# Optimization experiments

Hardware: AMD Instinct MI355X
Metric: run time of the kernel (lower is better)

The kernel has to match this reference:

```python
import jax, jax.numpy as jnp
import numpy as np

K = 20  # hard-coded in DGCNN.__init__

def _pd_neg(x):
    # negative squared pairwise distance, [B,N,C] -> [B,N,N]
    inner = jnp.einsum('bnc,bmc->bnm', x, x)
    sq = jnp.sum(x * x, axis=-1)
    return 2.0 * inner - sq[:, :, None] - sq[:, None, :]

def _knn(x):
    return jax.lax.top_k(_pd_neg(x), K)[1]  # [B,N,K]

def _edge_feat(x, idx):
    # x: [B,N,C], idx: [B,N,K] -> [B,N,K,2C] = concat(central, neighbor-central)
    nb = jax.vmap(lambda p, i: p[i])(x, idx)
    c = x[:, :, None, :]
    return jnp.concatenate([jnp.broadcast_to(c, nb.shape), nb - c], axis=-1)

def _conv(x, w, b, act=True):
    # 1x1 Conv2d == per-point linear; BN at inference with init stats is identity
    y = jnp.einsum('...c,cd->...d', x, w) + b
    return jax.nn.relu(y) if act else y

def _forward(x, tw1, tb1, tw2, tb2, tw3, tb3, tfw1, tfb1, tfw2, tfb2, txw, txb,
             e1w1, e1b1, e1w2, e1b2, e2w1, e2b1, e2w2, e2b2, e3w1, e3b1,
             c1w, c1b, c2w, c2b, c3w, c3b, c4w, c4b):
    pts = x[:, :, :3]
    # spatial transform net on edge features of raw xyz
    ef = _edge_feat(pts, _knn(pts))                      # [B,N,K,6]
    t = _conv(_conv(ef, tw1, tb1), tw2, tb2)
    t = jnp.max(t, axis=2)                               # max over neighbors
    t = _conv(t, tw3, tb3)                               # [B,N,1024]
    t = jnp.max(t, axis=1)                               # global maxpool -> [B,1024]
    t = jax.nn.relu(t @ tfw1 + tfb1)
    t = jax.nn.relu(t @ tfw2 + tfb2)
    xf = (t @ txw + txb).reshape(-1, 3, 3)
    p = jnp.einsum('bnc,bcd->bnd', pts, xf)              # transformed points
    # EdgeConv 1
    ef = _edge_feat(p, _knn(p))                          # [B,N,K,6]
    x1 = jnp.max(_conv(_conv(ef, e1w1, e1b1), e1w2, e1b2), axis=2)   # [B,N,64]
    # EdgeConv 2
    ef = _edge_feat(x1, _knn(x1))                        # [B,N,K,128]
    x2 = jnp.max(_conv(_conv(ef, e2w1, e2b1), e2w2, e2b2), axis=2)
    # EdgeConv 3
    ef = _edge_feat(x2, _knn(x2))
    x3 = jnp.max(_conv(ef, e3w1, e3b1), axis=2)
    # global feature + per-point head
    net = _conv(jnp.concatenate([x1, x2, x3], axis=-1), c1w, c1b)    # [B,N,1024]
    g = jnp.max(net, axis=1, keepdims=True)              # maxpool over all points
    g = jnp.broadcast_to(g, (g.shape[0], x1.shape[1], g.shape[2]))
    net = jnp.concatenate([g, x1, x2, x3], axis=-1)      # [B,N,1216]
    net = _conv(net, c2w, c2b)
    net = _conv(net, c3w, c3b)
    # dropout is identity at inference (training=False)
    return _conv(net, c4w, c4b, act=False)               # [B,N,num_classes]

def setup_inputs():
    keys = iter(jax.random.split(jax.random.key(0), 64))
    def w(*shape):
        return jax.random.normal(next(keys), shape, jnp.float32) / np.float32(np.sqrt(shape[0]))
    def b(n):
        return 0.01 * jax.random.normal(next(keys), (n,), jnp.float32)
    B, N, F = 4, 4096, 6
    d = dict(x=jax.random.normal(next(keys), (B, N, F), jnp.float32))
    d.update(tw1=w(6, 64), tb1=b(64), tw2=w(64, 128), tb2=b(128), tw3=w(128, 1024), tb3=b(1024),
             tfw1=w(1024, 512), tfb1=b(512), tfw2=w(512, 256), tfb2=b(256),
             txw=0.01 * w(256, 9), txb=jnp.eye(3, dtype=jnp.float32).reshape(9))
    d.update(e1w1=w(6, 64), e1b1=b(64), e1w2=w(64, 64), e1b2=b(64),
             e2w1=w(128, 64), e2b1=b(64), e2w2=w(64, 64), e2b2=b(64),
             e3w1=w(128, 64), e3b1=b(64))
    d.update(c1w=w(192, 1024), c1b=b(1024), c2w=w(1216, 512), c2b=b(512),
             c3w=w(512, 256), c3b=b(256), c4w=w(256, 2), c4b=b(2))
    return d

def reference(x, tw1, tb1, tw2, tb2, tw3, tb3, tfw1, tfb1, tfw2, tfb2, txw, txb,
              e1w1, e1b1, e1w2, e1b2, e2w1, e2b1, e2w2, e2b2, e3w1, e3b1,
              c1w, c1b, c2w, c2b, c3w, c3b, c4w, c4b):
    return _forward(x, tw1, tb1, tw2, tb2, tw3, tb3, tfw1, tfb1, tfw2, tfb2, txw, txb,
                    e1w1, e1b1, e1w2, e1b2, e2w1, e2b1, e2w2, e2b2, e3w1, e3b1,
                    c1w, c1b, c2w, c2b, c3w, c3b, c4w, c4b)
```

## Files before the change

kernel.cpp:

```cpp
#include <hip/hip_runtime.h>

#define Nn 4096
#define KK 20
#define BN 16384

typedef __attribute__((ext_vector_type(8))) short bf16x8;
typedef __attribute__((ext_vector_type(4))) float f32x4;

__device__ __forceinline__ unsigned short f2bf(float f) {
  unsigned int x = __float_as_uint(f);
  return (unsigned short)((x + 0x7fffu + ((x >> 16) & 1u)) >> 16);
}
__device__ __forceinline__ float bf2f(unsigned short u) {
  return __uint_as_float(((unsigned int)u) << 16);
}

#define INS5(dd, tt)                                                         \
  if (dd > m5) {                                                             \
    if (dd > m3) {                                                           \
      if (dd > m1) { m5=m4;t5=t4; m4=m3;t4=t3; m3=m2;t3=t2; m2=m1;t2=t1; m1=dd;t1=tt; } \
      else if (dd > m2) { m5=m4;t5=t4; m4=m3;t4=t3; m3=m2;t3=t2; m2=dd;t2=tt; } \
      else { m5=m4;t5=t4; m4=m3;t4=t3; m3=dd;t3=tt; }                        \
    } else if (dd > m4) { m5=m4;t5=t4; m4=dd;t4=tt; }                        \
    else { m5=dd; t5=tt; }                                                   \
  }

__global__ void k_pts(const float* __restrict__ x, float* __restrict__ pts) {
  int i = blockIdx.x * 256 + threadIdx.x;
  if (i < BN * 3) {
    int pt = i / 3, c = i - 3 * pt;
    pts[i] = x[pt * 6 + c];
  }
}

__global__ void k_cvtT(const float* __restrict__ src, unsigned short* __restrict__ dst,
                       int N, int K, int ldn, int row0) {
  int i = blockIdx.x * 256 + threadIdx.x;
  if (i >= N * K) return;
  int n = i / K, k = i - n * K;
  dst[i] = f2bf(src[(size_t)(row0 + k) * ldn + n]);
}

__global__ void k_cvtT3(const float* __restrict__ src, unsigned short* __restrict__ h,
                        unsigned short* __restrict__ m, unsigned short* __restrict__ l,
                        int N, int K, int ldn) {
  int i = blockIdx.x * 256 + threadIdx.x;
  if (i >= N * K) return;
  int n = i / K, k = i - n * K;
  float x = src[(size_t)k * ldn + n];
  unsigned short hh = f2bf(x); float xh = bf2f(hh);
  unsigned short mm = f2bf(x - xh); float xm = bf2f(mm);
  unsigned short ll = f2bf(x - xh - xm);
  h[i] = hh; m[i] = mm; l[i] = ll;
}

__global__ void k_tv3(const float* __restrict__ part, const float* __restrict__ bias,
                      unsigned short* __restrict__ h, unsigned short* __restrict__ m,
                      unsigned short* __restrict__ l) {
  int i = blockIdx.x * 256 + threadIdx.x;
  if (i >= 16 * 1024) return;
  int row = i >> 10, col = i & 1023;
  float v = 0.f;
  if (row < 4) {
    float mx = -INFINITY;
#pragma unroll 8
    for (int s = 0; s < 32; ++s) mx = fmaxf(mx, part[((size_t)row * 32 + s) * 1024 + col]);
    v = fmaxf(mx + bias[col], 0.f);
  }
  unsigned short hh = f2bf(v); float xh = bf2f(hh);
  unsigned short mm = f2bf(v - xh); float xm = bf2f(mm);
  unsigned short ll = f2bf(v - xh - xm);
  h[i] = hh; m[i] = mm; l[i] = ll;
}

__global__ void k_pad3(const float* __restrict__ src, int rows, int cols,
                       unsigned short* __restrict__ h, unsigned short* __restrict__ m,
                       unsigned short* __restrict__ l) {
  int i = blockIdx.x * 256 + threadIdx.x;
  if (i >= 16 * cols) return;
  int row = i / cols, col = i - row * cols;
  float v = (row < rows) ? src[(size_t)row * cols + col] : 0.f;
  unsigned short hh = f2bf(v); float xh = bf2f(hh);
  unsigned short mm = f2bf(v - xh); float xm = bf2f(mm);
  unsigned short ll = f2bf(v - xh - xm);
  h[i] = hh; m[i] = mm; l[i] = ll;
}

template <int N, int K, int SEG>
__global__ __launch_bounds__(256) void k_gemmSK(const unsigned short* __restrict__ Ah,
                                                const unsigned short* __restrict__ Am,
                                                const unsigned short* __restrict__ Al,
                                                const unsigned short* __restrict__ Bh,
                                                const unsigned short* __restrict__ Bm,
                                                const unsigned short* __restrict__ Bl,
                                                float* __restrict__ partial) {
  constexpr int KSEG = K / SEG;
  constexpr int KS = KSEG / 32;
  int t = threadIdx.x;
  int wv = t >> 6, lane = t & 63;
  int quad = lane >> 4, l16 = lane & 15;
  int bx = blockIdx.x;
  int nb = bx / SEG, seg = bx - nb * SEG;
  int col = nb * 64 + wv * 16 + l16;
  int k0 = seg * KSEG;
  size_t wo = (size_t)col * K + k0 + quad * 8;
  size_t ao = (size_t)l16 * K + k0 + quad * 8;
  f32x4 acc = {0.f, 0.f, 0.f, 0.f};
#pragma unroll
  for (int s = 0; s < KS; ++s) {
    bf16x8 xh = *(const bf16x8*)(Ah + ao + s * 32);
    bf16x8 xm = *(const bf16x8*)(Am + ao + s * 32);
    bf16x8 xl = *(const bf16x8*)(Al + ao + s * 32);
    bf16x8 wh = *(const bf16x8*)(Bh + wo + s * 32);
    bf16x8 wm = *(const bf16x8*)(Bm + wo + s * 32);
    bf16x8 wl = *(const bf16x8*)(Bl + wo + s * 32);
    acc = __builtin_amdgcn_mfma_f32_16x16x32_bf16(xh, wh, acc, 0, 0, 0);
    acc = __builtin_amdgcn_mfma_f32_16x16x32_bf16(xh, wm, acc, 0, 0, 0);
    acc = __builtin_amdgcn_mfma_f32_16x16x32_bf16(xm, wh, acc, 0, 0, 0);
    acc = __builtin_amdgcn_mfma_f32_16x16x32_bf16(xh, wl, acc, 0, 0, 0);
    acc = __builtin_amdgcn_mfma_f32_16x16x32_bf16(xl, wh, acc, 0, 0, 0);
    acc = __builtin_amdgcn_mfma_f32_16x16x32_bf16(xm, wm, acc, 0, 0, 0);
  }
  if (quad == 0) {
#pragma unroll
    for (int r = 0; r < 4; ++r)
      partial[((size_t)seg * 4 + r) * N + col] = acc[r];
  }
}

__global__ void k_redS(const float* __restrict__ partial, const float* __restrict__ bias,
                       float* __restrict__ outp, int N, int SEG, int relu) {
  int i = blockIdx.x * 256 + threadIdx.x;
  if (i >= 4 * N) return;
  int r = i / N, c = i - r * N;
  float s = 0.f;
  for (int seg = 0; seg < SEG; ++seg) s += partial[((size_t)seg * 4 + r) * N + c];
  if (bias) s += bias[c];
  if (relu) s = fmaxf(s, 0.f);
  outp[(size_t)r * N + c] = s;
}

__global__ __launch_bounds__(256) void k_fc3p(const float* __restrict__ h2, const float* __restrict__ txw,
                                              const float* __restrict__ txb, const float* __restrict__ pts,
                                              float* __restrict__ p) {
  __shared__ float sh2[256];
  __shared__ float sxf[9];
  int t = threadIdx.x;
  int b = blockIdx.x;
  sh2[t] = h2[(size_t)b * 256 + t];
  __syncthreads();
  if (t < 9) {
    float acc = txb[t];
    for (int j = 0; j < 256; ++j) acc = fmaf(sh2[j], txw[j * 9 + t], acc);
    sxf[t] = acc;
  }
  __syncthreads();
  for (int n = t; n < Nn; n += 256) {
    const float* pr = pts + ((size_t)b * Nn + n) * 3;
    float a0 = pr[0], a1 = pr[1], a2 = pr[2];
    float* po = p + ((size_t)b * Nn + n) * 3;
#pragma unroll
    for (int d = 0; d < 3; ++d) po[d] = a0 * sxf[d] + a1 * sxf[3 + d] + a2 * sxf[6 + d];
  }
}

__device__ __forceinline__ float dist4(const float4* __restrict__ tile4, int c,
                                       float qx, float qy, float qz, float qsq) {
  float4 v = tile4[c];
  float dot = fmaf(qx, v.x, fmaf(qy, v.y, qz * v.z));
  return 2.0f * dot - qsq - v.w;
}

__global__ __launch_bounds__(1024) void k_knn3(const float* __restrict__ src, int* __restrict__ idx) {
  __shared__ float4 tile4[Nn];
  int t = threadIdx.x;
  int wave = t >> 6, lane = t & 63;
  int g = blockIdx.x * 16 + wave;
  int b = g >> 12, n = g & (Nn - 1);
  const float* base = src + (size_t)b * Nn * 3;
  for (int e = t; e < Nn; e += 1024) {
    float x = base[e * 3], y = base[e * 3 + 1], z = base[e * 3 + 2];
    tile4[e] = make_float4(x, y, z, fmaf(x, x, fmaf(y, y, z * z)));
  }
  __syncthreads();
  float4 q4 = tile4[n];
  float qx = q4.x, qy = q4.y, qz = q4.z, qsq = q4.w;
  float m1 = -INFINITY, m2 = -INFINITY, m3 = -INFINITY, m4 = -INFINITY, m5 = -INFINITY;
  int t1 = 0, t2 = 0, t3 = 0, t4 = 0, t5 = 0;
#pragma unroll 4
  for (int tt = 0; tt < 64; ++tt) {
    float dd = dist4(tile4, (tt << 6) + lane, qx, qy, qz, qsq);
    INS5(dd, tt)
  }
  unsigned long long removed = 0ull;
  int cnt = 5;
  int sel = 0;
#pragma unroll 1
  for (int k = 0; k < 20; ++k) {
    float v = m1; int ci = (t1 << 6) | lane;
    float mx = v;
#pragma unroll
    for (int off = 32; off; off >>= 1) mx = fmaxf(mx, __shfl_xor(mx, off, 64));
    int cand = (v == mx) ? ci : 0x7FFFFFFF;
#pragma unroll
    for (int off = 32; off; off >>= 1) cand = min(cand, __shfl_xor(cand, off, 64));
    if (k == lane) sel = cand;
    if (cand == ci) {
      removed |= 1ull << t1;
      if (cnt > 1) { m1 = m2; t1 = t2; m2 = m3; t2 = t3; m3 = m4; t3 = t4; m4 = m5; t4 = t5; --cnt; }
      else {
        m1 = -INFINITY; m2 = -INFINITY; m3 = -INFINITY; m4 = -INFINITY; m5 = -INFINITY;
        t1 = 0; t2 = 0; t3 = 0; t4 = 0; t5 = 0;
#pragma unroll 1
        for (int tt = 0; tt < 64; ++tt) {
          if ((removed >> tt) & 1ull) continue;
          float dd = dist4(tile4, (tt << 6) + lane, qx, qy, qz, qsq);
          INS5(dd, tt)
        }
        cnt = 5;
      }
    }
  }
  if (lane < 20) idx[(size_t)g * KK + lane] = sel;
}

__global__ void k_sqnorm(const float* __restrict__ src, float* __restrict__ out) {
  int g = blockIdx.x * 256 + threadIdx.x;
  if (g >= BN) return;
  const float4* r = (const float4*)(src + (size_t)g * 64);
  float s = 0.f;
#pragma unroll
  for (int j = 0; j < 16; ++j) { float4 v = r[j]; s += v.x * v.x + v.y * v.y + v.z * v.z + v.w * v.w; }
  out[g] = s;
}

__device__ __forceinline__ void topk_d5(const float (&d)[64],
                                        float m1, int t1, float m2, int t2, float m3, int t3,
                                        float m4, int t4, float m5, int t5,
                                        int lane, int* __restrict__ op) {
  unsigned long long removed = 0ull;
  int cnt = 5;
  int sel = 0;
#pragma unroll 1
  for (int k = 0; k < 20; ++k) {
    float v = m1; int ci = (t1 << 6) | lane;
    float mx = v;
#pragma unroll
    for (int off = 32; off; off >>= 1) mx = fmaxf(mx, __shfl_xor(mx, off, 64));
    int cand = (v == mx) ? ci : 0x7FFFFFFF;
#pragma unroll
    for (int off = 32; off; off >>= 1) cand = min(cand, __shfl_xor(cand, off, 64));
    if (k == lane) sel = cand;
    if (cand == ci) {
      removed |= 1ull << t1;
      if (cnt > 1) { m1 = m2; t1 = t2; m2 = m3; t2 = t3; m3 = m4; t3 = t4; m4 = m5; t4 = t5; --cnt; }
      else {
        m1 = -INFINITY; m2 = -INFINITY; m3 = -INFINITY; m4 = -INFINITY; m5 = -INFINITY;
        t1 = 0; t2 = 0; t3 = 0; t4 = 0; t5 = 0;
#pragma unroll 1
        for (int tt = 0; tt < 64; ++tt) {
          if ((removed >> tt) & 1ull) continue;
          float dd = d[tt];
          INS5(dd, tt)
        }
        cnt = 5;
      }
    }
  }
  if (lane < 20) op[lane] = sel;
}

__global__ __launch_bounds__(1024) void k_dsel(const unsigned short* __restrict__ Xh,
                                               const unsigned short* __restrict__ Xm,
                                               const unsigned short* __restrict__ Xl,
                                               const float* __restrict__ sq,
                                               int* __restrict__ idx) {
  __shared__ float sD[16 * 1028];
  int t = threadIdx.x;
  int wave = t >> 6, lane = t & 63;
  int quad = lane >> 4, l16 = lane & 15;
  int blk = blockIdx.x;
  int b = blk >> 8, rs = blk & 255;
  int r0 = rs * 16;
  const size_t base = (size_t)b * Nn * 64;
  const float* sqb = sq + b * Nn;
  bf16x8 ah[2], am[2], al[2];
#pragma unroll
  for (int ks = 0; ks < 2; ++ks) {
    size_t ra = base + (size_t)(r0 + l16) * 64 + ks * 32 + quad * 8;
    ah[ks] = *(const bf16x8*)(Xh + ra);
    am[ks] = *(const bf16x8*)(Xm + ra);
    al[ks] = *(const bf16x8*)(Xl + ra);
  }
  float sqr[4];
#pragma unroll
  for (int r = 0; r < 4; ++r) sqr[r] = sqb[r0 + quad * 4 + r];
  float d[64];
  float m1 = -INFINITY, m2 = -INFINITY, m3 = -INFINITY, m4 = -INFINITY, m5 = -INFINITY;
  int t1 = 0, t2 = 0, t3 = 0, t4 = 0, t5 = 0;
#pragma unroll
  for (int ch = 0; ch < 4; ++ch) {
#pragma unroll
    for (int tt = 0; tt < 4; ++tt) {
      int cc = wave * 64 + tt * 16;
      int cb = ch * 1024 + cc;
      f32x4 acc = {0.f, 0.f, 0.f, 0.f};
#pragma unroll
      for (int ks = 0; ks < 2; ++ks) {
        size_t rb = base + (size_t)(cb + l16) * 64 + ks * 32 + quad * 8;
        bf16x8 bh = *(const bf16x8*)(Xh + rb);
        bf16x8 bm = *(const bf16x8*)(Xm + rb);
        bf16x8 bl = *(const bf16x8*)(Xl + rb);
        acc = __builtin_amdgcn_mfma_f32_16x16x32_bf16(ah[ks], bh, acc, 0, 0, 0);
        acc = __builtin_amdgcn_mfma_f32_16x16x32_bf16(ah[ks], bm, acc, 0, 0, 0);
        acc = __builtin_amdgcn_mfma_f32_16x16x32_bf16(am[ks], bh, acc, 0, 0, 0);
        acc = __builtin_amdgcn_mfma_f32_16x16x32_bf16(ah[ks], bl, acc, 0, 0, 0);
        acc = __builtin_amdgcn_mfma_f32_16x16x32_bf16(al[ks], bh, acc, 0, 0, 0);
        acc = __builtin_amdgcn_mfma_f32_16x16x32_bf16(am[ks], bm, acc, 0, 0, 0);
      }
      float sqc = sqb[cb + l16];
#pragma unroll
      for (int r = 0; r < 4; ++r)
        sD[(quad * 4 + r) * 1028 + cc + l16] = 2.0f * acc[r] - sqr[r] - sqc;
    }
    __syncthreads();
#pragma unroll
    for (int jj = 0; jj < 16; ++jj) {
      int tt = ch * 16 + jj;
      float dd = sD[wave * 1028 + jj * 64 + lane];
      d[tt] = dd;
      INS5(dd, tt)
    }
    __syncthreads();
  }
  topk_d5(d, m1, t1, m2, t2, m3, t3, m4, t4, m5, t5, lane,
          idx + (size_t)(b * Nn + r0 + wave) * KK);
}

__global__ __launch_bounds__(256) void k_uv3(const float* __restrict__ pts, const float* __restrict__ w1,
                                             const float* __restrict__ b1, float* __restrict__ uvb) {
  __shared__ float sw[384];
  __shared__ float sb[64];
  int t = threadIdx.x;
  for (int e = t; e < 384; e += 256) sw[e] = w1[e];
  if (t < 64) sb[t] = b1[t];
  __syncthreads();
  int pl = t >> 6, c = t & 63;
  int p = blockIdx.x * 4 + pl;
  const float* pr = pts + (size_t)p * 3;
  float x0 = pr[0], x1 = pr[1], x2 = pr[2];
  float wb0 = sw[192 + c], wb1 = sw[256 + c], wb2 = sw[320 + c];
  float v = x0 * wb0 + x1 * wb1 + x2 * wb2;
  float u = sb[c] + x0 * (sw[c] - wb0) + x1 * (sw[64 + c] - wb1) + x2 * (sw[128 + c] - wb2);
  uvb[(size_t)p * 128 + c] = u;
  uvb[(size_t)p * 128 + 64 + c] = v;
}

__global__ void k_prepD(const float* __restrict__ w1, float* __restrict__ Md) {
  int i = blockIdx.x * 256 + threadIdx.x;
  if (i >= 8192) return;
  int j = i >> 7, c = i & 127;
  Md[i] = (c < 64) ? (w1[j * 64 + c] - w1[(64 + j) * 64 + c]) : w1[(64 + j) * 64 + (c - 64)];
}

__global__ __launch_bounds__(256) void k_uv(const float* __restrict__ x2, const float* __restrict__ Md,
                                            const float* __restrict__ bias, float* __restrict__ uv) {
  __shared__ float sM[8192];
  __shared__ float sx[32 * 68];
  int t = threadIdx.x;
  for (int e = t; e < 8192; e += 256) sM[e] = Md[e];
  int p0 = blockIdx.x * 32;
  for (int e = t; e < 512; e += 256) {
    int r = e >> 4, c4 = e & 15;
    *(float4*)(sx + r * 68 + c4 * 4) = *(const float4*)(x2 + (size_t)(p0 + r) * 64 + c4 * 4);
  }
  __syncthreads();
  int c = t & 127, rg = t >> 7;
  float badd = (c < 64) ? bias[c] : 0.f;
  float accv[16];
#pragma unroll
  for (int r = 0; r < 16; ++r) accv[r] = 0.f;
#pragma unroll
  for (int jc = 0; jc < 8; ++jc) {
    float mreg[8];
#pragma unroll
    for (int q = 0; q < 8; ++q) mreg[q] = sM[(jc * 8 + q) * 128 + c];
#pragma unroll
    for (int r = 0; r < 16; ++r) {
      const float* xr = sx + (rg * 16 + r) * 68 + jc * 8;
      float4 a = *(const float4*)xr, bb = *(const float4*)(xr + 4);
      float s = accv[r];
      s = fmaf(a.x, mreg[0], s); s = fmaf(a.y, mreg[1], s);
      s = fmaf(a.z, mreg[2], s); s = fmaf(a.w, mreg[3], s);
      s = fmaf(bb.x, mreg[4], s); s = fmaf(bb.y, mreg[5], s);
      s = fmaf(bb.z, mreg[6], s); s = fmaf(bb.w, mreg[7], s);
      accv[r] = s;
    }
  }
#pragma unroll
  for (int r = 0; r < 16; ++r)
    uv[(size_t)(p0 + rg * 16 + r) * 128 + c] = accv[r] + badd;
}

template <int NOUT, bool WRITEF, bool SPLIT3, bool CAT>
__global__ __launch_bounds__(256, 4) void k_econv(const float* __restrict__ uv,
                                                  const int* __restrict__ idx,
                                                  const unsigned short* __restrict__ W2h,
                                                  const unsigned short* __restrict__ W2m,
                                                  const unsigned short* __restrict__ W2l,
                                                  const float* __restrict__ b2,
                                                  float* __restrict__ outF,
                                                  unsigned short* __restrict__ oh,
                                                  unsigned short* __restrict__ om,
                                                  unsigned short* __restrict__ ol,
                                                  unsigned short* __restrict__ ocat,
                                                  int catoff) {
  __shared__ unsigned short y3[4][3][20 * 72];
  int t = threadIdx.x;
  int wv = t >> 6, lane = t & 63;
  int quad = lane >> 4, l16 = lane & 15;
  int p0 = blockIdx.x * 4;
  int p = p0 + wv;
  size_t nbase = (size_t)(p >> 12) * Nn;
  constexpr int CT = NOUT / 64;
  bf16x8 wfh[CT][2], wfm[CT][2], wfl[CT][2];
#pragma unroll
  for (int ct = 0; ct < CT; ++ct)
#pragma unroll
    for (int ks = 0; ks < 2; ++ks) {
      size_t wo = (size_t)(wv * (CT * 16) + ct * 16 + l16) * 64 + ks * 32 + quad * 8;
      wfh[ct][ks] = *(const bf16x8*)(W2h + wo);
      wfm[ct][ks] = *(const bf16x8*)(W2m + wo);
      wfl[ct][ks] = *(const bf16x8*)(W2l + wo);
    }
  const int* ip = idx + (size_t)p * KK;
  float u = uv[(size_t)p * 128 + lane];
  unsigned short* yh = y3[wv][0];
  unsigned short* ym = y3[wv][1];
  unsigned short* yl = y3[wv][2];
  float vv[20];
#pragma unroll
  for (int k = 0; k < 20; ++k) {
    int nb = ip[k];
    vv[k] = uv[(nbase + nb) * 128 + 64 + lane];
  }
#pragma unroll
  for (int k = 0; k < 20; ++k) {
    float y = fmaxf(u + vv[k], 0.f);
    unsigned short hh = f2bf(y); float fh = bf2f(hh);
    unsigned short mm = f2bf(y - fh); float fm = bf2f(mm);
    unsigned short ll = f2bf(y - fh - fm);
    yh[k * 72 + lane] = hh;
    ym[k * 72 + lane] = mm;
    yl[k * 72 + lane] = ll;
  }
  __syncthreads();
#pragma unroll 1
  for (int pp = 0; pp < 4; ++pp) {
    const unsigned short* ph0 = y3[pp][0];
    const unsigned short* pm0 = y3[pp][1];
    const unsigned short* pl0 = y3[pp][2];
    f32x4 acc[CT][2];
#pragma unroll
    for (int ct = 0; ct < CT; ++ct) {
      acc[ct][0] = (f32x4){0.f, 0.f, 0.f, 0.f};
      acc[ct][1] = (f32x4){0.f, 0.f, 0.f, 0.f};
    }
#pragma unroll
    for (int ks = 0; ks < 2; ++ks) {
      bf16x8 ah[2], am[2], al[2];
#pragma unroll
      for (int mt = 0; mt < 2; ++mt) {
        int row = mt * 16 + l16;
        int rr = (row < 20) ? row : 0;
        int aoff = rr * 72 + ks * 32 + quad * 8;
        ah[mt] = *(const bf16x8*)(ph0 + aoff);
        am[mt] = *(const bf16x8*)(pm0 + aoff);
        al[mt] = *(const bf16x8*)(pl0 + aoff);
      }
#pragma unroll
      for (int ct = 0; ct < CT; ++ct)
#pragma unroll
        for (int mt = 0; mt < 2; ++mt) {
          f32x4 a = acc[ct][mt];
          a = __builtin_amdgcn_mfma_f32_16x16x32_bf16(ah[mt], wfh[ct][ks], a, 0, 0, 0);
          a = __builtin_amdgcn_mfma_f32_16x16x32_bf16(ah[mt], wfm[ct][ks], a, 0, 0, 0);
          a = __builtin_amdgcn_mfma_f32_16x16x32_bf16(am[mt], wfh[ct][ks], a, 0, 0, 0);
          a = __builtin_amdgcn_mfma_f32_16x16x32_bf16(ah[mt], wfl[ct][ks], a, 0, 0, 0);
          a = __builtin_amdgcn_mfma_f32_16x16x32_bf16(al[mt], wfh[ct][ks], a, 0, 0, 0);
// ... 62 lines not shown
#pragma unroll
  for (int s = 0; s < KS; ++s) bfr[s] = *(const bf16x8*)(wrow + s * 32);
  const unsigned short* Ab = A + ((size_t)b * Nn + ns * 128 + l16) * K + quad * 8;
  float rmax = -INFINITY;
#pragma unroll 2
  for (int mt = 0; mt < 8; ++mt) {
    const unsigned short* ar = Ab + (size_t)mt * 16 * K;
    f32x4 acc = {0.f, 0.f, 0.f, 0.f};
#pragma unroll
    for (int s = 0; s < KS; ++s) {
      bf16x8 af = *(const bf16x8*)(ar + s * 32);
      acc = __builtin_amdgcn_mfma_f32_16x16x32_bf16(af, bfr[s], acc, 0, 0, 0);
    }
    rmax = fmaxf(rmax, fmaxf(fmaxf(acc[0], acc[1]), fmaxf(acc[2], acc[3])));
  }
  rmax = fmaxf(rmax, __shfl_xor(rmax, 16, 64));
  rmax = fmaxf(rmax, __shfl_xor(rmax, 32, 64));
  if (quad == 0) outp[((size_t)b * 32 + ns) * 1024 + n0 + l16] = rmax;
}

template <int K>
__global__ __launch_bounds__(256) void k_mgemm3s(const unsigned short* __restrict__ Ah,
                                                 const unsigned short* __restrict__ Am,
                                                 const unsigned short* __restrict__ Al,
                                                 const unsigned short* __restrict__ Bh,
                                                 const unsigned short* __restrict__ Bm,
                                                 const unsigned short* __restrict__ Bl,
                                                 float* __restrict__ outp) {
  constexpr int KS = K / 32;
  int t = threadIdx.x;
  int wv = t >> 6, lane = t & 63;
  int quad = lane >> 4, l16 = lane & 15;
  int blk = blockIdx.x;
  int b = blk >> 9, cb = (blk >> 5) & 15, ns = blk & 31;
  int n0 = cb * 64 + wv * 16;
  bf16x8 wh[KS], wm[KS], wl[KS];
  size_t wo = (size_t)(n0 + l16) * K + quad * 8;
#pragma unroll
  for (int s = 0; s < KS; ++s) {
    wh[s] = *(const bf16x8*)(Bh + wo + s * 32);
    wm[s] = *(const bf16x8*)(Bm + wo + s * 32);
    wl[s] = *(const bf16x8*)(Bl + wo + s * 32);
  }
  size_t ao = ((size_t)b * Nn + ns * 128 + l16) * K + quad * 8;
  float rmax = -INFINITY;
#pragma unroll 1
  for (int mt = 0; mt < 8; ++mt) {
    size_t ar = ao + (size_t)mt * 16 * K;
    f32x4 acc = {0.f, 0.f, 0.f, 0.f};
#pragma unroll
    for (int s = 0; s < KS; ++s) {
      bf16x8 xh = *(const bf16x8*)(Ah + ar + s * 32);
      bf16x8 xm = *(const bf16x8*)(Am + ar + s * 32);
      bf16x8 xl = *(const bf16x8*)(Al + ar + s * 32);
      acc = __builtin_amdgcn_mfma_f32_16x16x32_bf16(xh, wh[s], acc, 0, 0, 0);
      acc = __builtin_amdgcn_mfma_f32_16x16x32_bf16(xh, wm[s], acc, 0, 0, 0);
      acc = __builtin_amdgcn_mfma_f32_16x16x32_bf16(xm, wh[s], acc, 0, 0, 0);
      acc = __builtin_amdgcn_mfma_f32_16x16x32_bf16(xh, wl[s], acc, 0, 0, 0);
      acc = __builtin_amdgcn_mfma_f32_16x16x32_bf16(xl, wh[s], acc, 0, 0, 0);
      acc = __builtin_amdgcn_mfma_f32_16x16x32_bf16(xm, wm[s], acc, 0, 0, 0);
    }
    rmax = fmaxf(rmax, fmaxf(fmaxf(acc[0], acc[1]), fmaxf(acc[2], acc[3])));
  }
  rmax = fmaxf(rmax, __shfl_xor(rmax, 16, 64));
  rmax = fmaxf(rmax, __shfl_xor(rmax, 32, 64));
  if (quad == 0) outp[((size_t)b * 32 + ns) * 1024 + n0 + l16] = rmax;
}

__global__ __launch_bounds__(256) void k_final(const unsigned short* __restrict__ xcat,
                                               const float* __restrict__ gc,
                                               const float* __restrict__ c2b,
                                               const unsigned short* __restrict__ c2wT,
                                               const unsigned short* __restrict__ c3wT,
                                               const float* __restrict__ c3b,
                                               const float* __restrict__ c4w, const float* __restrict__ c4b,
                                               float* __restrict__ out) {
  __shared__ unsigned short z5[16 * 520];
  __shared__ float z2[16 * 260];
  int t = threadIdx.x;
  int wv = t >> 6, lane = t & 63;
  int quad = lane >> 4, l16 = lane & 15;
  int p0 = blockIdx.x * 16;
  int b = p0 >> 12;
  bf16x8 a1[6];
  const unsigned short* ar = xcat + (size_t)(p0 + l16) * 192 + quad * 8;
#pragma unroll
  for (int s = 0; s < 6; ++s) a1[s] = *(const bf16x8*)(ar + s * 32);
#pragma unroll 1
  for (int ntw = 0; ntw < 8; ++ntw) {
    int col = wv * 128 + ntw * 16 + l16;
    float bias = gc[(size_t)b * 512 + col] + c2b[col];
    f32x4 acc = {bias, bias, bias, bias};
    const unsigned short* wr = c2wT + (size_t)col * 192 + quad * 8;
#pragma unroll
    for (int s = 0; s < 6; ++s) {
      bf16x8 bfr = *(const bf16x8*)(wr + s * 32);
      acc = __builtin_amdgcn_mfma_f32_16x16x32_bf16(a1[s], bfr, acc, 0, 0, 0);
    }
#pragma unroll
    for (int r = 0; r < 4; ++r)
      z5[(quad * 4 + r) * 520 + col] = f2bf(fmaxf(acc[r], 0.f));
  }
  __syncthreads();
  bf16x8 a2[16];
#pragma unroll
  for (int s = 0; s < 16; ++s) a2[s] = *(const bf16x8*)(z5 + l16 * 520 + s * 32 + quad * 8);
#pragma unroll 1
  for (int ntw = 0; ntw < 4; ++ntw) {
    int col = wv * 64 + ntw * 16 + l16;
    float bias = c3b[col];
    f32x4 acc = {bias, bias, bias, bias};
    const unsigned short* wr = c3wT + (size_t)col * 512 + quad * 8;
#pragma unroll
    for (int s = 0; s < 16; ++s) {
      bf16x8 bfr = *(const bf16x8*)(wr + s * 32);
      acc = __builtin_amdgcn_mfma_f32_16x16x32_bf16(a2[s], bfr, acc, 0, 0, 0);
    }
#pragma unroll
    for (int r = 0; r < 4; ++r)
      z2[(quad * 4 + r) * 260 + col] = fmaxf(acc[r], 0.f);
  }
  __syncthreads();
  if (t < 32) {
    int m = t >> 1, e = t & 1;
    float acc = c4b[e];
    const float* zr = z2 + m * 260;
    for (int j = 0; j < 256; ++j) acc = fmaf(zr[j], c4w[j * 2 + e], acc);
    out[(size_t)(p0 + m) * 2 + e] = acc;
  }
}

extern "C" void kernel_launch(void* const* d_in, const int* in_sizes, int n_in,
                              void* d_out, int out_size, void* d_ws, size_t ws_size,
                              hipStream_t stream) {
  const float* xin = (const float*)d_in[0];
  const float* W[30];
  for (int i = 0; i < 30; ++i) W[i] = (const float*)d_in[i + 1];

  float* ws = (float*)d_ws;
  size_t off = 0;
  float* pts   = ws + off; off += (size_t)BN * 3;
  float* p     = ws + off; off += (size_t)BN * 3;
  int*   idx   = (int*)(ws + off); off += (size_t)BN * KK;
  float* sq    = ws + off; off += BN;
  float* dpart = ws + off; off += 4 * 32 * 1024;
  float* h1    = ws + off; off += 4 * 512;
  float* h2b   = ws + off; off += 4 * 256;
  float* x1    = ws + off; off += (size_t)BN * 64;
  float* x2    = ws + off; off += (size_t)BN * 64;
  float* gpart = ws + off; off += 4 * 32 * 1024;
  float* gc    = ws + off; off += 4 * 512;
  float* uvb   = ws + off; off += (size_t)BN * 128;
  float* partial = ws + off; off += 16 * 4 * 512;
  unsigned short* xcat = (unsigned short*)(ws + off); off += (size_t)BN * 96;
  unsigned short* c1wT = (unsigned short*)(ws + off); off += 98304;
  unsigned short* c2wT = (unsigned short*)(ws + off); off += 49152;
  unsigned short* c3wT = (unsigned short*)(ws + off); off += 65536;
  unsigned short* w3Th = (unsigned short*)(ws + off); off += 65536;
  unsigned short* w3Tm = (unsigned short*)(ws + off); off += 65536;
  unsigned short* w3Tl = (unsigned short*)(ws + off); off += 65536;
  unsigned short* tw2h = (unsigned short*)(ws + off); off += 4096;
  unsigned short* tw2m = (unsigned short*)(ws + off); off += 4096;
  unsigned short* tw2l = (unsigned short*)(ws + off); off += 4096;
  unsigned short* e1h  = (unsigned short*)(ws + off); off += 2048;
  unsigned short* e1m  = (unsigned short*)(ws + off); off += 2048;
  unsigned short* e1l  = (unsigned short*)(ws + off); off += 2048;
  unsigned short* e2h  = (unsigned short*)(ws + off); off += 2048;
  unsigned short* e2m  = (unsigned short*)(ws + off); off += 2048;
  unsigned short* e2l  = (unsigned short*)(ws + off); off += 2048;
  unsigned short* xsh  = (unsigned short*)(ws + off); off += 524288;
  unsigned short* xsm  = (unsigned short*)(ws + off); off += 524288;
  unsigned short* xsl  = (unsigned short*)(ws + off); off += 524288;
  float* MdC   = ws + off; off += 8192;
  float* MdD   = ws + off; off += 8192;
  unsigned short* fw1h = (unsigned short*)(ws + off); off += 262144;
  unsigned short* fw1m = (unsigned short*)(ws + off); off += 262144;
  unsigned short* fw1l = (unsigned short*)(ws + off); off += 262144;
  unsigned short* cw2h = (unsigned short*)(ws + off); off += 262144;
  unsigned short* cw2m = (unsigned short*)(ws + off); off += 262144;
  unsigned short* cw2l = (unsigned short*)(ws + off); off += 262144;
  unsigned short* fw2h = (unsigned short*)(ws + off); off += 65536;
  unsigned short* fw2m = (unsigned short*)(ws + off); off += 65536;
  unsigned short* fw2l = (unsigned short*)(ws + off); off += 65536;
  unsigned short* tvh  = (unsigned short*)(ws + off); off += 8192;
  unsigned short* tvm  = (unsigned short*)(ws + off); off += 8192;
  unsigned short* tvl  = (unsigned short*)(ws + off); off += 8192;
  unsigned short* h13h = (unsigned short*)(ws + off); off += 4096;
  unsigned short* h13m = (unsigned short*)(ws + off); off += 4096;
  unsigned short* h13l = (unsigned short*)(ws + off); off += 4096;
  float* Dbuf  = ws + off; off += (size_t)Nn * Nn;
  unsigned short* t3h = (unsigned short*)Dbuf;
  unsigned short* t3m = t3h + (size_t)BN * 128;
  unsigned short* t3l = t3m + (size_t)BN * 128;

  k_cvtT<<<dim3(768), dim3(256), 0, stream>>>(W[22], c1wT, 1024, 192, 1024, 0);
  k_cvtT<<<dim3(384), dim3(256), 0, stream>>>(W[24], c2wT, 512, 192, 512, 1024);
  k_cvtT<<<dim3(512), dim3(256), 0, stream>>>(W[26], c3wT, 256, 512, 256, 0);
  k_cvtT3<<<dim3(512), dim3(256), 0, stream>>>(W[4], w3Th, w3Tm, w3Tl, 1024, 128, 1024);
  k_cvtT3<<<dim3(32), dim3(256), 0, stream>>>(W[2], tw2h, tw2m, tw2l, 128, 64, 128);
  k_cvtT3<<<dim3(16), dim3(256), 0, stream>>>(W[14], e1h, e1m, e1l, 64, 64, 64);
  k_cvtT3<<<dim3(16), dim3(256), 0, stream>>>(W[18], e2h, e2m, e2l, 64, 64, 64);
  k_cvtT3<<<dim3(2048), dim3(256), 0, stream>>>(W[6], fw1h, fw1m, fw1l, 512, 1024, 512);
  k_cvtT3<<<dim3(2048), dim3(256), 0, stream>>>(W[24], cw2h, cw2m, cw2l, 512, 1024, 512);
  k_cvtT3<<<dim3(512), dim3(256), 0, stream>>>(W[8], fw2h, fw2m, fw2l, 256, 512, 256);
  k_prepD<<<dim3(32), dim3(256), 0, stream>>>(W[16], MdC);
  k_prepD<<<dim3(32), dim3(256), 0, stream>>>(W[20], MdD);

  k_pts<<<dim3(192), dim3(256), 0, stream>>>(xin, pts);

  k_knn3<<<dim3(1024), dim3(1024), 0, stream>>>(pts, idx);
  k_uv3<<<dim3(4096), dim3(256), 0, stream>>>(pts, W[0], W[1], uvb);
  k_econv<128, false, true, false><<<dim3(4096), dim3(256), 0, stream>>>(
      uvb, idx, tw2h, tw2m, tw2l, W[3], nullptr, t3h, t3m, t3l, nullptr, 0);
  k_mgemm3s<128><<<dim3(2048), dim3(256), 0, stream>>>(t3h, t3m, t3l, w3Th, w3Tm, w3Tl, dpart);
  k_tv3<<<dim3(64), dim3(256), 0, stream>>>(dpart, W[5], tvh, tvm, tvl);
  k_gemmSK<512, 1024, 16><<<dim3(128), dim3(256), 0, stream>>>(tvh, tvm, tvl, fw1h, fw1m, fw1l, partial);
  k_redS<<<dim3(8), dim3(256), 0, stream>>>(partial, W[7], h1, 512, 16, 1);
  k_pad3<<<dim3(32), dim3(256), 0, stream>>>(h1, 4, 512, h13h, h13m, h13l);
  k_gemmSK<256, 512, 8><<<dim3(32), dim3(256), 0, stream>>>(h13h, h13m, h13l, fw2h, fw2m, fw2l, partial);
  k_redS<<<dim3(4), dim3(256), 0, stream>>>(partial, W[9], h2b, 256, 8, 1);
  k_fc3p<<<dim3(4), dim3(256), 0, stream>>>(h2b, W[10], W[11], pts, p);

  k_knn3<<<dim3(1024), dim3(1024), 0, stream>>>(p, idx);
  k_uv3<<<dim3(4096), dim3(256), 0, stream>>>(p, W[12], W[13], uvb);
  k_econv<64, true, true, true><<<dim3(4096), dim3(256), 0, stream>>>(
      uvb, idx, e1h, e1m, e1l, W[15], x1, xsh, xsm, xsl, xcat, 0);
  k_sqnorm<<<dim3(64), dim3(256), 0, stream>>>(x1, sq);
  k_dsel<<<dim3(1024), dim3(1024), 0, stream>>>(xsh, xsm, xsl, sq, idx);
  k_uv<<<dim3(512), dim3(256), 0, stream>>>(x1, MdC, W[17], uvb);
  k_econv<64, true, true, true><<<dim3(4096), dim3(256), 0, stream>>>(
      uvb, idx, e2h, e2m, e2l, W[19], x2, xsh, xsm, xsl, xcat, 64);
  k_sqnorm<<<dim3(64), dim3(256), 0, stream>>>(x2, sq);
  k_dsel<<<dim3(1024), dim3(1024), 0, stream>>>(xsh, xsm, xsl, sq, idx);
  k_uv<<<dim3(512), dim3(256), 0, stream>>>(x2, MdD, W[21], uvb);
  k_gmax<<<dim3(4096), dim3(256), 0, stream>>>(uvb, idx, xcat);

  k_mgemm<192><<<dim3(2048), dim3(256), 0, stream>>>(xcat, c1wT, gpart);
  k_tv3<<<dim3(64), dim3(256), 0, stream>>>(gpart, W[23], tvh, tvm, tvl);
  k_gemmSK<512, 1024, 16><<<dim3(128), dim3(256), 0, stream>>>(tvh, tvm, tvl, cw2h, cw2m, cw2l, partial);
  k_redS<<<dim3(8), dim3(256), 0, stream>>>(partial, nullptr, gc, 512, 16, 0);
  k_final<<<dim3(1024), dim3(256), 0, stream>>>(xcat, gc, W[25], c2wT, c3wT,
                                                W[27], W[28], W[29], (float*)d_out);
}
```

Baseline: 1.276 ms.

## Split 64-dim kNN into column-quarter top-k kernels plus a merge pass

The fused distance and top-20 selection kernel for the 64-channel EdgeConv layers is replaced by two kernels. The first computes distances for 8 rows against a quarter of the columns in 512-thread blocks and writes per-quarter top-20 candidates. The second merges the 80 candidates per row into the final top-20. This adds parallelism, shrinks per-thread register arrays (16 instead of 64 values) and makes the rescan cheaper. In exchange, half the MFMA rows are wasted and candidates take an extra global round trip.

```diff
diff --git a/kernel.cpp b/kernel.cpp
--- a/kernel.cpp
+++ b/kernel.cpp
@@ -234,13 +234,70 @@
   out[g] = s;
 }
 
-__device__ __forceinline__ void topk_d5(const float (&d)[64],
-                                        float m1, int t1, float m2, int t2, float m3, int t3,
-                                        float m4, int t4, float m5, int t5,
-                                        int lane, int* __restrict__ op) {
-  unsigned long long removed = 0ull;
+__global__ __launch_bounds__(512) void k_dq(const unsigned short* __restrict__ Xh,
+                                            const unsigned short* __restrict__ Xm,
+                                            const unsigned short* __restrict__ Xl,
+                                            const float* __restrict__ sq,
+                                            float* __restrict__ cval,
+                                            int* __restrict__ cidx) {
+  __shared__ float sD[8 * 1028];
+  int t = threadIdx.x;
+  int wave = t >> 6, lane = t & 63;
+  int quad = lane >> 4, l16 = lane & 15;
+  int blk = blockIdx.x;
+  int b = blk >> 11, rs = (blk >> 2) & 511, qtr = blk & 3;
+  int r0 = rs * 8, q0 = qtr * 1024;
+  const size_t base = (size_t)b * Nn * 64;
+  const float* sqb = sq + b * Nn;
+  bf16x8 ah[2], am[2], al[2];
+#pragma unroll
+  for (int ks = 0; ks < 2; ++ks) {
+    size_t ra = base + (size_t)(r0 + (l16 & 7)) * 64 + ks * 32 + quad * 8;
+    ah[ks] = *(const bf16x8*)(Xh + ra);
+    am[ks] = *(const bf16x8*)(Xm + ra);
+    al[ks] = *(const bf16x8*)(Xl + ra);
+  }
+  float sqr[4];
+#pragma unroll
+  for (int r = 0; r < 4; ++r) sqr[r] = sqb[r0 + ((quad * 4 + r) & 7)];
+#pragma unroll
+  for (int tt = 0; tt < 8; ++tt) {
+    int cc = wave * 128 + tt * 16;
+    int cb = q0 + cc;
+    f32x4 acc = {0.f, 0.f, 0.f, 0.f};
+#pragma unroll
+    for (int ks = 0; ks < 2; ++ks) {
+      size_t rb = base + (size_t)(cb + l16) * 64 + ks * 32 + quad * 8;
+      bf16x8 bh = *(const bf16x8*)(Xh + rb);
+      bf16x8 bm = *(const bf16x8*)(Xm + rb);
+      bf16x8 bl = *(const bf16x8*)(Xl + rb);
+      acc = __builtin_amdgcn_mfma_f32_16x16x32_bf16(ah[ks], bh, acc, 0, 0, 0);
+      acc = __builtin_amdgcn_mfma_f32_16x16x32_bf16(ah[ks], bm, acc, 0, 0, 0);
+      acc = __builtin_amdgcn_mfma_f32_16x16x32_bf16(am[ks], bh, acc, 0, 0, 0);
+      acc = __builtin_amdgcn_mfma_f32_16x16x32_bf16(ah[ks], bl, acc, 0, 0, 0);
+      acc = __builtin_amdgcn_mfma_f32_16x16x32_bf16(al[ks], bh, acc, 0, 0, 0);
+      acc = __builtin_amdgcn_mfma_f32_16x16x32_bf16(am[ks], bm, acc, 0, 0, 0);
+    }
+    float sqc = sqb[cb + l16];
+    if (quad < 2) {
+#pragma unroll
+      for (int r = 0; r < 4; ++r)
+        sD[(quad * 4 + r) * 1028 + cc + l16] = 2.0f * acc[r] - sqr[r] - sqc;
+    }
+  }
+  __syncthreads();
+  float d[16];
+  float m1 = -INFINITY, m2 = -INFINITY, m3 = -INFINITY, m4 = -INFINITY, m5 = -INFINITY;
+  int t1 = 0, t2 = 0, t3 = 0, t4 = 0, t5 = 0;
+#pragma unroll
+  for (int jj = 0; jj < 16; ++jj) {
+    float dd = sD[wave * 1028 + jj * 64 + lane];
+    d[jj] = dd;
+    INS5(dd, jj)
+  }
+  unsigned removed = 0;
   int cnt = 5;
-  int sel = 0;
+  float selv = 0.f; int seli = 0;
 #pragma unroll 1
   for (int k = 0; k < 20; ++k) {
     float v = m1; int ci = (t1 << 6) | lane;
@@ -250,91 +307,59 @@
     int cand = (v == mx) ? ci : 0x7FFFFFFF;
 #pragma unroll
     for (int off = 32; off; off >>= 1) cand = min(cand, __shfl_xor(cand, off, 64));
-    if (k == lane) sel = cand;
+    if (k == lane) { selv = mx; seli = cand; }
     if (cand == ci) {
-      removed |= 1ull << t1;
+      removed |= 1u << t1;
       if (cnt > 1) { m1 = m2; t1 = t2; m2 = m3; t2 = t3; m3 = m4; t3 = t4; m4 = m5; t4 = t5; --cnt; }
       else {
         m1 = -INFINITY; m2 = -INFINITY; m3 = -INFINITY; m4 = -INFINITY; m5 = -INFINITY;
         t1 = 0; t2 = 0; t3 = 0; t4 = 0; t5 = 0;
-#pragma unroll 1
-        for (int tt = 0; tt < 64; ++tt) {
-          if ((removed >> tt) & 1ull) continue;
-          float dd = d[tt];
-          INS5(dd, tt)
+#pragma unroll
+        for (int tt = 0; tt < 16; ++tt) {
+          if (!((removed >> tt) & 1u)) {
+            float dd = d[tt];
+            INS5(dd, tt)
+          }
         }
         cnt = 5;
       }
     }
   }
-  if (lane < 20) op[lane] = sel;
-}
-
-__global__ __launch_bounds__(1024) void k_dsel(const unsigned short* __restrict__ Xh,
-                                               const unsigned short* __restrict__ Xm,
-                                               const unsigned short* __restrict__ Xl,
-                                               const float* __restrict__ sq,
-                                               int* __restrict__ idx) {
-  __shared__ float sD[16 * 1028];
+  if (lane < 20) {
+    size_t o = ((size_t)(b * Nn + r0 + wave) * 4 + qtr) * 20 + lane;
+    cval[o] = selv;
+    cidx[o] = q0 + seli;
+  }
+}
+
+__global__ __launch_bounds__(256) void k_dmerge(const float* __restrict__ cval,
+                                                const int* __restrict__ cidx,
+                                                int* __restrict__ idx) {
   int t = threadIdx.x;
   int wave = t >> 6, lane = t & 63;
-  int quad = lane >> 4, l16 = lane & 15;
-  int blk = blockIdx.x;
-  int b = blk >> 8, rs = blk & 255;
-  int r0 = rs * 16;
-  const size_t base = (size_t)b * Nn * 64;
-  const float* sqb = sq + b * Nn;
-  bf16x8 ah[2], am[2], al[2];
-#pragma unroll
-  for (int ks = 0; ks < 2; ++ks) {
-    size_t ra = base + (size_t)(r0 + l16) * 64 + ks * 32 + quad * 8;
-    ah[ks] = *(const bf16x8*)(Xh + ra);
-    am[ks] = *(const bf16x8*)(Xm + ra);
-    al[ks] = *(const bf16x8*)(Xl + ra);
-  }
-  float sqr[4];
-#pragma unroll
-  for (int r = 0; r < 4; ++r) sqr[r] = sqb[r0 + quad * 4 + r];
-  float d[64];
-  float m1 = -INFINITY, m2 = -INFINITY, m3 = -INFINITY, m4 = -INFINITY, m5 = -INFINITY;
-  int t1 = 0, t2 = 0, t3 = 0, t4 = 0, t5 = 0;
-#pragma unroll
-  for (int ch = 0; ch < 4; ++ch) {
-#pragma unroll
-    for (int tt = 0; tt < 4; ++tt) {
-      int cc = wave * 64 + tt * 16;
-      int cb = ch * 1024 + cc;
-      f32x4 acc = {0.f, 0.f, 0.f, 0.f};
-#pragma unroll
-      for (int ks = 0; ks < 2; ++ks) {
-        size_t rb = base + (size_t)(cb + l16) * 64 + ks * 32 + quad * 8;
-        bf16x8 bh = *(const bf16x8*)(Xh + rb);
-        bf16x8 bm = *(const bf16x8*)(Xm + rb);
-        bf16x8 bl = *(const bf16x8*)(Xl + rb);
-        acc = __builtin_amdgcn_mfma_f32_16x16x32_bf16(ah[ks], bh, acc, 0, 0, 0);
-        acc = __builtin_amdgcn_mfma_f32_16x16x32_bf16(ah[ks], bm, acc, 0, 0, 0);
-        acc = __builtin_amdgcn_mfma_f32_16x16x32_bf16(am[ks], bh, acc, 0, 0, 0);
-        acc = __builtin_amdgcn_mfma_f32_16x16x32_bf16(ah[ks], bl, acc, 0, 0, 0);
-        acc = __builtin_amdgcn_mfma_f32_16x16x32_bf16(al[ks], bh, acc, 0, 0, 0);
-        acc = __builtin_amdgcn_mfma_f32_16x16x32_bf16(am[ks], bm, acc, 0, 0, 0);
-      }
-      float sqc = sqb[cb + l16];
-#pragma unroll
-      for (int r = 0; r < 4; ++r)
-        sD[(quad * 4 + r) * 1028 + cc + l16] = 2.0f * acc[r] - sqr[r] - sqc;
-    }
-    __syncthreads();
-#pragma unroll
-    for (int jj = 0; jj < 16; ++jj) {
-      int tt = ch * 16 + jj;
-      float dd = sD[wave * 1028 + jj * 64 + lane];
-      d[tt] = dd;
-      INS5(dd, tt)
-    }
-    __syncthreads();
-  }
-  topk_d5(d, m1, t1, m2, t2, m3, t3, m4, t4, m5, t5, lane,
-          idx + (size_t)(b * Nn + r0 + wave) * KK);
+  int row = blockIdx.x * 4 + wave;
+  size_t o = (size_t)row * 80;
+  float v0 = cval[o + lane];
+  int i0 = cidx[o + lane];
+  float v1 = -INFINITY; int i1 = 0x7FFFFFFF;
+  if (lane < 16) { v1 = cval[o + 64 + lane]; i1 = cidx[o + 64 + lane]; }
+  if (v1 > v0 || (v1 == v0 && i1 < i0)) {
+    float tv = v0; v0 = v1; v1 = tv;
+    int ti = i0; i0 = i1; i1 = ti;
+  }
+  int sel = 0;
+#pragma unroll 1
+  for (int k = 0; k < 20; ++k) {
+    float mx = v0;
+#pragma unroll
+    for (int off = 32; off; off >>= 1) mx = fmaxf(mx, __shfl_xor(mx, off, 64));
+    int cand = (v0 == mx) ? i0 : 0x7FFFFFFF;
+#pragma unroll
+    for (int off = 32; off; off >>= 1) cand = min(cand, __shfl_xor(cand, off, 64));
+    if (k == lane) sel = cand;
+    if (cand == i0) { v0 = v1; i0 = i1; v1 = -INFINITY; i1 = 0x7FFFFFFF; }
+  }
+  if (lane < 20) idx[(size_t)row * KK + lane] = sel;
 }
 
 __global__ __launch_bounds__(256) void k_uv3(const float* __restrict__ pts, const float* __restrict__ w1,
@@ -743,6 +768,8 @@
   unsigned short* t3h = (unsigned short*)Dbuf;
   unsigned short* t3m = t3h + (size_t)BN * 128;
   unsigned short* t3l = t3m + (size_t)BN * 128;
+  float* cval  = Dbuf;
+  int*   cidxb = (int*)(Dbuf + (size_t)BN * 80);
 
   k_cvtT<<<dim3(768), dim3(256), 0, stream>>>(W[22], c1wT, 1024, 192, 1024, 0);
   k_cvtT<<<dim3(384), dim3(256), 0, stream>>>(W[24], c2wT, 512, 192, 512, 1024);
@@ -777,12 +804,14 @@
   k_econv<64, true, true, true><<<dim3(4096), dim3(256), 0, stream>>>(
       uvb, idx, e1h, e1m, e1l, W[15], x1, xsh, xsm, xsl, xcat, 0);
   k_sqnorm<<<dim3(64), dim3(256), 0, stream>>>(x1, sq);
-  k_dsel<<<dim3(1024), dim3(1024), 0, stream>>>(xsh, xsm, xsl, sq, idx);
+  k_dq<<<dim3(8192), dim3(512), 0, stream>>>(xsh, xsm, xsl, sq, cval, cidxb);
+  k_dmerge<<<dim3(4096), dim3(256), 0, stream>>>(cval, cidxb, idx);
   k_uv<<<dim3(512), dim3(256), 0, stream>>>(x1, MdC, W[17], uvb);
   k_econv<64, true, true, true><<<dim3(4096), dim3(256), 0, stream>>>(
       uvb, idx, e2h, e2m, e2l, W[19], x2, xsh, xsm, xsl, xcat, 64);
   k_sqnorm<<<dim3(64), dim3(256), 0, stream>>>(x2, sq);
-  k_dsel<<<dim3(1024), dim3(1024), 0, stream>>>(xsh, xsm, xsl, sq, idx);
+  k_dq<<<dim3(8192), dim3(512), 0, stream>>>(xsh, xsm, xsl, sq, cval, cidxb);
+  k_dmerge<<<dim3(4096), dim3(256), 0, stream>>>(cval, cidxb, idx);
   k_uv<<<dim3(512), dim3(256), 0, stream>>>(x2, MdD, W[21], uvb);
   k_gmax<<<dim3(4096), dim3(256), 0, stream>>>(uvb, idx, xcat);
 
```

Result: slower. 1.589 ms (+24.5%).

## Split kNN top-k selection into fast path plus rare-row fallback kernel

Applied to the files above, without the earlier changes.

The distance-select kernel no longer keeps a 64-entry per-lane distance array in registers for re-scanning. Each lane keeps only its top-5 candidates. If any lane runs out of candidates during the 20-way selection, the row is flagged through an atomic counter and list, and a new fallback kernel recomputes that full distance row in shared memory and redoes the exact selection. This is meant to cut register pressure and spilling in the common path, at the cost of a memset, an extra launch of mostly early-exiting blocks, and a fixed cap of 2048 rows that can be repaired.

```diff
diff --git a/kernel.cpp b/kernel.cpp
--- a/kernel.cpp
+++ b/kernel.cpp
@@ -3,6 +3,7 @@
 #define Nn 4096
 #define KK 20
 #define BN 16384
+#define FCAP 2048
 
 typedef __attribute__((ext_vector_type(8))) short bf16x8;
 typedef __attribute__((ext_vector_type(4))) float f32x4;
@@ -234,47 +235,13 @@
   out[g] = s;
 }
 
-__device__ __forceinline__ void topk_d5(const float (&d)[64],
-                                        float m1, int t1, float m2, int t2, float m3, int t3,
-                                        float m4, int t4, float m5, int t5,
-                                        int lane, int* __restrict__ op) {
-  unsigned long long removed = 0ull;
-  int cnt = 5;
-  int sel = 0;
-#pragma unroll 1
-  for (int k = 0; k < 20; ++k) {
-    float v = m1; int ci = (t1 << 6) | lane;
-    float mx = v;
-#pragma unroll
-    for (int off = 32; off; off >>= 1) mx = fmaxf(mx, __shfl_xor(mx, off, 64));
-    int cand = (v == mx) ? ci : 0x7FFFFFFF;
-#pragma unroll
-    for (int off = 32; off; off >>= 1) cand = min(cand, __shfl_xor(cand, off, 64));
-    if (k == lane) sel = cand;
-    if (cand == ci) {
-      removed |= 1ull << t1;
-      if (cnt > 1) { m1 = m2; t1 = t2; m2 = m3; t2 = t3; m3 = m4; t3 = t4; m4 = m5; t4 = t5; --cnt; }
-      else {
-        m1 = -INFINITY; m2 = -INFINITY; m3 = -INFINITY; m4 = -INFINITY; m5 = -INFINITY;
-        t1 = 0; t2 = 0; t3 = 0; t4 = 0; t5 = 0;
-#pragma unroll 1
-        for (int tt = 0; tt < 64; ++tt) {
-          if ((removed >> tt) & 1ull) continue;
-          float dd = d[tt];
-          INS5(dd, tt)
-        }
-        cnt = 5;
-      }
-    }
-  }
-  if (lane < 20) op[lane] = sel;
-}
-
-__global__ __launch_bounds__(1024) void k_dsel(const unsigned short* __restrict__ Xh,
-                                               const unsigned short* __restrict__ Xm,
-                                               const unsigned short* __restrict__ Xl,
-                                               const float* __restrict__ sq,
-                                               int* __restrict__ idx) {
+__global__ __launch_bounds__(1024) void k_dself(const unsigned short* __restrict__ Xh,
+                                                const unsigned short* __restrict__ Xm,
+                                                const unsigned short* __restrict__ Xl,
+                                                const float* __restrict__ sq,
+                                                int* __restrict__ flagc,
+                                                int* __restrict__ flagr,
+                                                int* __restrict__ idx) {
   __shared__ float sD[16 * 1028];
   int t = threadIdx.x;
   int wave = t >> 6, lane = t & 63;
@@ -295,7 +262,6 @@
   float sqr[4];
 #pragma unroll
   for (int r = 0; r < 4; ++r) sqr[r] = sqb[r0 + quad * 4 + r];
-  float d[64];
   float m1 = -INFINITY, m2 = -INFINITY, m3 = -INFINITY, m4 = -INFINITY, m5 = -INFINITY;
   int t1 = 0, t2 = 0, t3 = 0, t4 = 0, t5 = 0;
 #pragma unroll
@@ -328,13 +294,121 @@
     for (int jj = 0; jj < 16; ++jj) {
       int tt = ch * 16 + jj;
       float dd = sD[wave * 1028 + jj * 64 + lane];
-      d[tt] = dd;
       INS5(dd, tt)
     }
     __syncthreads();
   }
-  topk_d5(d, m1, t1, m2, t2, m3, t3, m4, t4, m5, t5, lane,
-          idx + (size_t)(b * Nn + r0 + wave) * KK);
+  int cnt = 5;
+  int sel = 0;
+  bool fail = false;
+#pragma unroll 1
+  for (int k = 0; k < 20; ++k) {
+    float v = m1; int ci = (t1 << 6) | lane;
+    float mx = v;
+#pragma unroll
+    for (int off = 32; off; off >>= 1) mx = fmaxf(mx, __shfl_xor(mx, off, 64));
+    int cand = (v == mx) ? ci : 0x7FFFFFFF;
+#pragma unroll
+    for (int off = 32; off; off >>= 1) cand = min(cand, __shfl_xor(cand, off, 64));
+    if (k == lane) sel = cand;
+    if (cand == ci) {
+      if (cnt > 1) { m1 = m2; t1 = t2; m2 = m3; t2 = t3; m3 = m4; t3 = t4; m4 = m5; t4 = t5; --cnt; }
+      else { fail = true; m1 = -INFINITY; }
+    }
+  }
+  int row = b * Nn + r0 + wave;
+  if (lane < 20) idx[(size_t)row * KK + lane] = sel;
+  unsigned long long fm = __ballot(fail);
+  if (fm != 0ull && lane == 0) {
+    int p = atomicAdd(flagc, 1);
+    if (p < FCAP) flagr[p] = row;
+  }
+}
+
+__global__ __launch_bounds__(1024) void k_dfix(const unsigned short* __restrict__ Xh,
+                                               const unsigned short* __restrict__ Xm,
+                                               const unsigned short* __restrict__ Xl,
+                                               const float* __restrict__ sq,
+                                               const int* __restrict__ flagc,
+                                               const int* __restrict__ flagr,
+                                               int* __restrict__ idx) {
+  __shared__ float sRow[Nn];
+  int nf = flagc[0]; if (nf > FCAP) nf = FCAP;
+  if ((int)blockIdx.x >= nf) return;
+  int row = flagr[blockIdx.x];
+  int b = row >> 12, r = row & (Nn - 1);
+  int t = threadIdx.x;
+  int wave = t >> 6, lane = t & 63;
+  int quad = lane >> 4, l16 = lane & 15;
+  const size_t base = (size_t)b * Nn * 64;
+  const float* sqb = sq + b * Nn;
+  bf16x8 ah[2], am[2], al[2];
+#pragma unroll
+  for (int ks = 0; ks < 2; ++ks) {
+    size_t ra = base + (size_t)r * 64 + ks * 32 + quad * 8;
+    ah[ks] = *(const bf16x8*)(Xh + ra);
+    am[ks] = *(const bf16x8*)(Xm + ra);
+    al[ks] = *(const bf16x8*)(Xl + ra);
+  }
+  float sqr = sqb[r];
+#pragma unroll 1
+  for (int tt = 0; tt < 16; ++tt) {
+    int cb = wave * 256 + tt * 16;
+    f32x4 acc = {0.f, 0.f, 0.f, 0.f};
+#pragma unroll
+    for (int ks = 0; ks < 2; ++ks) {
+      size_t rb = base + (size_t)(cb + l16) * 64 + ks * 32 + quad * 8;
+      bf16x8 bh = *(const bf16x8*)(Xh + rb);
+      bf16x8 bm = *(const bf16x8*)(Xm + rb);
+      bf16x8 bl = *(const bf16x8*)(Xl + rb);
+      acc = __builtin_amdgcn_mfma_f32_16x16x32_bf16(ah[ks], bh, acc, 0, 0, 0);
+      acc = __builtin_amdgcn_mfma_f32_16x16x32_bf16(ah[ks], bm, acc, 0, 0, 0);
+      acc = __builtin_amdgcn_mfma_f32_16x16x32_bf16(am[ks], bh, acc, 0, 0, 0);
+      acc = __builtin_amdgcn_mfma_f32_16x16x32_bf16(ah[ks], bl, acc, 0, 0, 0);
+      acc = __builtin_amdgcn_mfma_f32_16x16x32_bf16(al[ks], bh, acc, 0, 0, 0);
+      acc = __builtin_amdgcn_mfma_f32_16x16x32_bf16(am[ks], bm, acc, 0, 0, 0);
+    }
+    if (quad == 0) sRow[cb + l16] = 2.0f * acc[0] - sqr - sqb[cb + l16];
+  }
+  __syncthreads();
+  if (wave != 0) return;
+  float m1 = -INFINITY, m2 = -INFINITY, m3 = -INFINITY, m4 = -INFINITY, m5 = -INFINITY;
+  int t1 = 0, t2 = 0, t3 = 0, t4 = 0, t5 = 0;
+#pragma unroll 1
+  for (int tt = 0; tt < 64; ++tt) {
+    float dd = sRow[(tt << 6) | lane];
+    INS5(dd, tt)
+  }
+  unsigned long long removed = 0ull;
+  int cnt = 5;
+  int sel = 0;
+#pragma unroll 1
+  for (int k = 0; k < 20; ++k) {
+    float v = m1; int ci = (t1 << 6) | lane;
+    float mx = v;
+#pragma unroll
+    for (int off = 32; off; off >>= 1) mx = fmaxf(mx, __shfl_xor(mx, off, 64));
+    int cand = (v == mx) ? ci : 0x7FFFFFFF;
+#pragma unroll
+    for (int off = 32; off; off >>= 1) cand = min(cand, __shfl_xor(cand, off, 64));
+    if (k == lane) sel = cand;
+    if (cand == ci) {
+      removed |= 1ull << t1;
+      if (cnt > 1) { m1 = m2; t1 = t2; m2 = m3; t2 = t3; m3 = m4; t3 = t4; m4 = m5; t4 = t5; --cnt; }
+      else {
+        m1 = -INFINITY; m2 = -INFINITY; m3 = -INFINITY; m4 = -INFINITY; m5 = -INFINITY;
+        t1 = 0; t2 = 0; t3 = 0; t4 = 0; t5 = 0;
+#pragma unroll 1
+        for (int tt = 0; tt < 64; ++tt) {
+          if ((removed >> tt) & 1ull) continue;
+          float dd = sRow[(tt << 6) | lane];
+          INS5(dd, tt)
+        }
+        cnt = 5;
+      }
+    }
+  }
+  if (lane < 20) idx[(size_t)row * KK + lane] = sel;
 }
 
 __global__ __launch_bounds__(256) void k_uv3(const float* __restrict__ pts, const float* __restrict__ w1,
@@ -703,6 +777,8 @@
   float* gc    = ws + off; off += 4 * 512;
   float* uvb   = ws + off; off += (size_t)BN * 128;
   float* partial = ws + off; off += 16 * 4 * 512;
+  int*   flagc = (int*)(ws + off); off += 16;
+  int*   flagr = (int*)(ws + off); off += FCAP;
   unsigned short* xcat = (unsigned short*)(ws + off); off += (size_t)BN * 96;
   unsigned short* c1wT = (unsigned short*)(ws + off); off += 98304;
   unsigned short* c2wT = (unsigned short*)(ws + off); off += 49152;
@@ -777,12 +853,16 @@
   k_econv<64, true, true, true><<<dim3(4096), dim3(256), 0, stream>>>(
       uvb, idx, e1h, e1m, e1l, W[15], x1, xsh, xsm, xsl, xcat, 0);
   k_sqnorm<<<dim3(64), dim3(256), 0, stream>>>(x1, sq);
-  k_dsel<<<dim3(1024), dim3(1024), 0, stream>>>(xsh, xsm, xsl, sq, idx);
+  hipMemsetAsync(flagc, 0, sizeof(int), stream);
+  k_dself<<<dim3(1024), dim3(1024), 0, stream>>>(xsh, xsm, xsl, sq, flagc, flagr, idx);
+  k_dfix<<<dim3(FCAP), dim3(1024), 0, stream>>>(xsh, xsm, xsl, sq, flagc, flagr, idx);
   k_uv<<<dim3(512), dim3(256), 0, stream>>>(x1, MdC, W[17], uvb);
   k_econv<64, true, true, true><<<dim3(4096), dim3(256), 0, stream>>>(
       uvb, idx, e2h, e2m, e2l, W[19], x2, xsh, xsm, xsl, xcat, 64);
   k_sqnorm<<<dim3(64), dim3(256), 0, stream>>>(x2, sq);
-  k_dsel<<<dim3(1024), dim3(1024), 0, stream>>>(xsh, xsm, xsl, sq, idx);
+  hipMemsetAsync(flagc, 0, sizeof(int), stream);
+  k_dself<<<dim3(1024), dim3(1024), 0, stream>>>(xsh, xsm, xsl, sq, flagc, flagr, idx);
+  k_dfix<<<dim3(FCAP), dim3(1024), 0, stream>>>(xsh, xsm, xsl, sq, flagc, flagr, idx);
   k_uv<<<dim3(512), dim3(256), 0, stream>>>(x2, MdD, W[21], uvb);
   k_gmax<<<dim3(4096), dim3(256), 0, stream>>>(uvb, idx, xcat);
 
```

Result: slower. 1.389 ms (+8.9%).
